# Kernel optimization log

Measured on AMD Instinct MI355X. Metric: run time of the kernel, lower is better.

The kernel has to match this reference:

```python
import jax, jax.numpy as jnp
import numpy as np

B, NBLK, D, DY, NDIM, NMC, DH = 4096, 12, 2, 2, 24, 256, 100
SQRT3 = 3.0 ** 0.5
G2 = np.array([[1.0, 0.0], [0.5, SQRT3 / 2.0]], dtype=np.float32)
G = jnp.asarray(np.kron(np.eye(NBLK, dtype=np.float32), G2))  # (24,24) block-diag hexagonal generator
LOG_VOL = (NDIM // 2) * float(np.log(SQRT3 / 2.0))  # log sqrt(det(G G^T))


def _lin(x, w, b=None):
    y = x @ w.T
    return y if b is None else y + b


def _hex_quantize(y):
    # Exact nearest-point quantizer for the product-of-A2 (hexagonal) lattice.
    p = y.reshape(y.shape[:-1] + (NDIM // 2, 2))
    off = jnp.array([0.5, SQRT3 / 2.0], dtype=y.dtype)
    def rnd(q):  # round to rectangular sublattice Z x sqrt(3)Z
        return jnp.stack([jnp.round(q[..., 0]), jnp.round(q[..., 1] / SQRT3) * SQRT3], axis=-1)
    c0 = rnd(p)
    c1 = rnd(p - off) + off
    d0 = jnp.sum((p - c0) ** 2, axis=-1)
    d1 = jnp.sum((p - c1) ** 2, axis=-1)
    return jnp.where((d0 <= d1)[..., None], c0, c1).reshape(y.shape)


def _logits_cumulative(v, Hs, bs, fs):
    # compressai-style per-channel monotone cumulative network. v: (..., C) -> (..., C)
    v = v[..., None]  # (..., C, 1)
    for k in range(len(Hs)):
        v = jnp.einsum('coi,...ci->...co', jax.nn.softplus(Hs[k]), v) + bs[k][:, :, 0]
        if k < len(fs):
            v = v + jnp.tanh(fs[k][:, :, 0]) * jnp.tanh(v)
    return v[..., 0]


def setup_inputs() -> dict:
    key = jax.random.key(0)
    ks = iter(jax.random.split(key, 64))
    def nrm(shape, s=1.0):
        return jax.random.normal(next(ks), shape, jnp.float32) * s
    inp = {}
    inp['x'] = nrm((B, NBLK, D))
    inp['y_mean'] = nrm((NBLK, DY))
    inp['u'] = jax.random.uniform(next(ks), (NMC, NDIM), jnp.float32)
    inp['ga_w0'] = nrm((DH, D), D ** -0.5); inp['ga_b0'] = jnp.zeros((DH,), jnp.float32)
    inp['ga_w1'] = nrm((DH, DH), DH ** -0.5); inp['ga_b1'] = jnp.zeros((DH,), jnp.float32)
    inp['ga_w2'] = nrm((DY, DH), DH ** -0.5); inp['ga_b2'] = jnp.zeros((DY,), jnp.float32)
    inp['gs_w0'] = nrm((DH, DY), DY ** -0.5); inp['gs_b0'] = jnp.zeros((DH,), jnp.float32)
    inp['gs_w1'] = nrm((DH, DH), DH ** -0.5); inp['gs_b1'] = jnp.zeros((DH,), jnp.float32)
    inp['gs_w2'] = nrm((D, DH), DH ** -0.5); inp['gs_b2'] = jnp.zeros((D,), jnp.float32)
    inp['gac_w0'] = nrm((DH, NDIM), NDIM ** -0.5)
    inp['gac_w1'] = nrm((DH, DH), DH ** -0.5)
    inp['gac_w2'] = nrm((NDIM, DH), DH ** -0.5)
    inp['gsc_w0'] = nrm((DH, NDIM), NDIM ** -0.5)
    inp['gsc_w1'] = nrm((DH, DH), DH ** -0.5)
    inp['gsc_w2'] = nrm((NDIM, DH), DH ** -0.5)
    # factorized-prior cumulative params, layer dims 1->3->3->3->3->1
    inp['eb_H0'] = nrm((NDIM, 3, 1), 0.5)
    inp['eb_H1'] = nrm((NDIM, 3, 3), 0.5)
    inp['eb_H2'] = nrm((NDIM, 3, 3), 0.5)
    inp['eb_H3'] = nrm((NDIM, 3, 3), 0.5)
    inp['eb_H4'] = nrm((NDIM, 1, 3), 0.5)
    inp['eb_b0'] = nrm((NDIM, 3, 1), 0.5)
    inp['eb_b1'] = nrm((NDIM, 3, 1), 0.5)
    inp['eb_b2'] = nrm((NDIM, 3, 1), 0.5)
    inp['eb_b3'] = nrm((NDIM, 3, 1), 0.5)
    inp['eb_b4'] = nrm((NDIM, 1, 1), 0.5)
    inp['eb_a0'] = nrm((NDIM, 3, 1), 0.5)
    inp['eb_a1'] = nrm((NDIM, 3, 1), 0.5)
    inp['eb_a2'] = nrm((NDIM, 3, 1), 0.5)
    inp['eb_a3'] = nrm((NDIM, 3, 1), 0.5)
    return inp


def reference(x, y_mean, u, ga_w0, ga_b0, ga_w1, ga_b1, ga_w2, ga_b2,
              gs_w0, gs_b0, gs_w1, gs_b1, gs_w2, gs_b2,
              gac_w0, gac_w1, gac_w2, gsc_w0, gsc_w1, gsc_w2,
              eb_H0, eb_H1, eb_H2, eb_H3, eb_H4,
              eb_b0, eb_b1, eb_b2, eb_b3, eb_b4,
              eb_a0, eb_a1, eb_a2, eb_a3):
    lrelu, sp = jax.nn.leaky_relu, jax.nn.softplus
    # analysis transform g_a: (B, 12, 2) -> (B, 12, dy)
    y1 = _lin(lrelu(_lin(lrelu(_lin(x, ga_w0, ga_b0)), ga_w1, ga_b1)), ga_w2, ga_b2)
    # EMA zero-mean update (buffer assignment => no gradient through the mean)
    ym = jax.lax.stop_gradient(0.05 * y_mean + 0.95 * jnp.mean(y1, axis=0))
    y1 = (y1 - ym).reshape(B, NDIM)
    # coupled analysis transform g_a_c (Softplus MLP, no bias)
    y1 = _lin(sp(_lin(sp(_lin(y1, gac_w0)), gac_w1)), gac_w2)
    # quasi-uniform samples from the Voronoi cell of the lattice origin
    u2 = u @ G
    u2 = u2 - _hex_quantize(u2)
    # lattice quantization with straight-through estimator
    y_q = _hex_quantize(y1)
    y_hat = y1 + jax.lax.stop_gradient(y_q - y1)
    # Monte-Carlo log-likelihood over the Voronoi cell with factorized prior density
    Hs = (eb_H0, eb_H1, eb_H2, eb_H3, eb_H4)
    bs = (eb_b0, eb_b1, eb_b2, eb_b3, eb_b4)
    fs = (eb_a0, eb_a1, eb_a2, eb_a3)
    pts = y_hat[:, None, :] + u2[None, :, :]  # (B, NMC, NDIM)
    def cdf(p):
        return jax.nn.sigmoid(_logits_cumulative(p, Hs, bs, fs))
    _, pdf = jax.jvp(cdf, (pts,), (jnp.ones_like(pts),))  # density = d/dx cdf(x)
    logp = jnp.sum(jnp.log(pdf + 1e-9), axis=-1)  # (B, NMC)
    lik = jax.scipy.special.logsumexp(logp, axis=1) - jnp.log(jnp.float32(NMC)) + LOG_VOL  # (B,)
    # synthesis transforms
    y_hat1 = _lin(sp(_lin(sp(_lin(y_hat, gsc_w0)), gsc_w1)), gsc_w2).reshape(B, NBLK, DY) + ym
    x_hat = _lin(lrelu(_lin(lrelu(_lin(y_hat1, gs_w0, gs_b0)), gs_w1, gs_b1)), gs_w2, gs_b2)
    return (x_hat, lik)
```

## Files before the change

### kernel.cpp

```cpp
#include <hip/hip_runtime.h>
#include <hip/hip_bf16.h>
#include <math.h>
#include <limits.h>

constexpr int NB    = 4096;
constexpr int ROWS2 = NB * 12;
constexpr int G2_BLOCKS = ROWS2 / 64;
constexpr int TBL_CAP = 64;
constexpr int KBASE   = -32;

constexpr size_t WS_Y1    = 0;
constexpr size_t WS_YHAT  = 98304;
constexpr size_t WS_YHAT1 = 196608;
constexpr size_t WS_YM    = 294912;
constexpr size_t WS_U2T   = 294936;
constexpr size_t WS_EB    = 301080;
constexpr size_t WS_PART  = 302472;
constexpr size_t WS_W1T   = 320904;
constexpr size_t WS_TBL   = 372104;
constexpr size_t WS_END   = WS_TBL + 24 * TBL_CAP * 256;

constexpr float STEP_ODD = 0.8660254037844386f;
constexpr float INV_ODD  = 1.1547005383792517f;

__device__ __forceinline__ float lrelu(float x) { return x >= 0.f ? x : 0.01f * x; }
__device__ __forceinline__ float rcp_fast(float x) { return __builtin_amdgcn_rcpf(x); }

__device__ __forceinline__ float tanh_fast(float x) {
    float xx = fminf(fmaxf(x, -15.f), 15.f);
    float e = __expf(xx + xx);
    return fmaf(-2.f, rcp_fast(e + 1.f), 1.f);
}
__device__ __forceinline__ float splus(float x) {
    return fmaxf(x, 0.f) + __logf(1.f + __expf(-fabsf(x)));
}
__device__ __forceinline__ float splus_precise(float x) {
    return fmaxf(x, 0.f) + log1pf(expf(-fabsf(x)));
}

__device__ __forceinline__ void fma4(float4& a, float h, const float4& w) {
    a.x = fmaf(h, w.x, a.x); a.y = fmaf(h, w.y, a.y);
    a.z = fmaf(h, w.z, a.z); a.w = fmaf(h, w.w, a.w);
}

__device__ __forceinline__ void hexq(float p0, float p1, float& q0, float& q1) {
    const float S3 = 1.7320508075688772f;
    const float H3 = 0.8660254037844386f;
    float c00 = rintf(p0);
    float c01 = rintf(p1 / S3) * S3;
    float c10 = rintf(p0 - 0.5f) + 0.5f;
    float c11 = rintf((p1 - H3) / S3) * S3 + H3;
    float d0 = (p0 - c00) * (p0 - c00) + (p1 - c01) * (p1 - c01);
    float d1 = (p0 - c10) * (p0 - c10) + (p1 - c11) * (p1 - c11);
    bool take0 = d0 <= d1;
    q0 = take0 ? c00 : c10;
    q1 = take0 ? c01 : c11;
}

__device__ __forceinline__ float logpdf_ch(const float* __restrict__ P, float p) {
    float w00 = P[0], w01 = P[1], w02 = P[2];
    float z0 = fmaf(w00, p, P[3]);
    float z1 = fmaf(w01, p, P[4]);
    float z2 = fmaf(w02, p, P[5]);
    float a0 = P[6], a1 = P[7], a2 = P[8];
    float e0 = tanh_fast(z0), e1 = tanh_fast(z1), e2 = tanh_fast(z2);
    float h0 = fmaf(a0, e0, z0), h1 = fmaf(a1, e1, z1), h2 = fmaf(a2, e2, z2);
    float t0 = w00 * fmaf(a0, fmaf(-e0, e0, 1.f), 1.f);
    float t1 = w01 * fmaf(a1, fmaf(-e1, e1, 1.f), 1.f);
    float t2 = w02 * fmaf(a2, fmaf(-e2, e2, 1.f), 1.f);

#define EB_LAYER(O)                                                            \
    {                                                                          \
        float z0n = fmaf(P[O+0], h0, fmaf(P[O+1], h1, fmaf(P[O+2], h2, P[O+9])));  \
        float z1n = fmaf(P[O+3], h0, fmaf(P[O+4], h1, fmaf(P[O+5], h2, P[O+10]))); \
        float z2n = fmaf(P[O+6], h0, fmaf(P[O+7], h1, fmaf(P[O+8], h2, P[O+11]))); \
        float s0 = fmaf(P[O+0], t0, fmaf(P[O+1], t1, P[O+2] * t2));            \
        float s1 = fmaf(P[O+3], t0, fmaf(P[O+4], t1, P[O+5] * t2));            \
        float s2 = fmaf(P[O+6], t0, fmaf(P[O+7], t1, P[O+8] * t2));            \
        float g0 = P[O+12], g1 = P[O+13], g2 = P[O+14];                        \
        float q0 = tanh_fast(z0n), q1 = tanh_fast(z1n), q2 = tanh_fast(z2n);   \
        h0 = fmaf(g0, q0, z0n); h1 = fmaf(g1, q1, z1n); h2 = fmaf(g2, q2, z2n); \
        t0 = s0 * fmaf(g0, fmaf(-q0, q0, 1.f), 1.f);                           \
        t1 = s1 * fmaf(g1, fmaf(-q1, q1, 1.f), 1.f);                           \
        t2 = s2 * fmaf(g2, fmaf(-q2, q2, 1.f), 1.f);                           \
    }
    EB_LAYER(9)
    EB_LAYER(24)
    EB_LAYER(39)
#undef EB_LAYER

    float L = fmaf(P[54], h0, fmaf(P[55], h1, fmaf(P[56], h2, P[57])));
    float T = fmaf(P[54], t0, fmaf(P[55], t1, P[56] * t2));
    float Lc = fminf(fmaxf(L, -30.f), 30.f);
    float sg = rcp_fast(1.f + __expf(-Lc));
    float pdf = sg * (1.f - sg) * T;
    return __logf(pdf + 1e-9f);
}

__global__ __launch_bounds__(256) void k_prep(
    const float* __restrict__ H0p, const float* __restrict__ H1p,
    const float* __restrict__ H2p, const float* __restrict__ H3p,
    const float* __restrict__ H4p,
    const float* __restrict__ b0p, const float* __restrict__ b1p,
    const float* __restrict__ b2p, const float* __restrict__ b3p,
    const float* __restrict__ b4p,
    const float* __restrict__ a0p, const float* __restrict__ a1p,
    const float* __restrict__ a2p, const float* __restrict__ a3p,
    const float* __restrict__ u,
    const float* __restrict__ w1ga, const float* __restrict__ w1gac,
    const float* __restrict__ w1gsc, const float* __restrict__ w1gs,
    float* __restrict__ eb, float* __restrict__ u2t,
    float* __restrict__ w1t)
{
    int tid = threadIdx.x;
    if (blockIdx.x > 0) {
        int t = blockIdx.x - 1;
        int m = t / 50;
        int o = (t % 50) * 256 + tid;
        int k = o >> 7, i = o & 127;
        const float* src = (m == 0) ? w1ga : (m == 1) ? w1gac
                         : (m == 2) ? w1gsc : w1gs;
        w1t[m * 12800 + o] = (i < 100) ? src[i * 100 + k] : 0.f;
        return;
    }
    if (tid < 24) {
        int c = tid;
        float* P = eb + c * 58;
        for (int j = 0; j < 3; ++j) P[j]      = splus_precise(H0p[c*3+j]);
        for (int j = 0; j < 3; ++j) P[3+j]    = b0p[c*3+j];
        for (int j = 0; j < 3; ++j) P[6+j]    = tanhf(a0p[c*3+j]);
        for (int j = 0; j < 9; ++j) P[9+j]    = splus_precise(H1p[c*9+j]);
        for (int j = 0; j < 3; ++j) P[18+j]   = b1p[c*3+j];
        for (int j = 0; j < 3; ++j) P[21+j]   = tanhf(a1p[c*3+j]);
        for (int j = 0; j < 9; ++j) P[24+j]   = splus_precise(H2p[c*9+j]);
        for (int j = 0; j < 3; ++j) P[33+j]   = b2p[c*3+j];
        for (int j = 0; j < 3; ++j) P[36+j]   = tanhf(a2p[c*3+j]);
        for (int j = 0; j < 9; ++j) P[39+j]   = splus_precise(H3p[c*9+j]);
        for (int j = 0; j < 3; ++j) P[48+j]   = b3p[c*3+j];
        for (int j = 0; j < 3; ++j) P[51+j]   = tanhf(a3p[c*3+j]);
        for (int j = 0; j < 3; ++j) P[54+j]   = splus_precise(H4p[c*3+j]);
        P[57] = b4p[c];
    }
    int m = tid;
    if (m < 256) {
        for (int j = 0; j < 12; ++j) {
            float a  = u[m*24 + 2*j];
            float bb = u[m*24 + 2*j + 1];
            float p0 = fmaf(0.5f, bb, a);
            float p1 = 0.8660254037844386f * bb;
            float q0, q1; hexq(p0, p1, q0, q1);
            u2t[(2*j)   * 256 + m] = p0 - q0;
            u2t[(2*j+1) * 256 + m] = p1 - q1;
        }
    }
}

template <int MEAN>
__device__ __forceinline__ void gemm2_body(
    int bid,
    const float* __restrict__ in,
    const float* __restrict__ w0, const float* __restrict__ b0,
    const float* __restrict__ w1t,
    const float* __restrict__ b1, const float* __restrict__ w2,
    const float* __restrict__ b2,
    float* __restrict__ out, float* __restrict__ partial)
{
    __shared__ alignas(16) float shT[100 * 64];
    __shared__ float S[64][2];

    int tid = threadIdx.x;
    int row0 = bid * 64;

    int lrow = tid & 63, jg = tid >> 6;
    float2 xv = ((const float2*)in)[row0 + lrow];
#pragma unroll
    for (int jj = 0; jj < 25; ++jj) {
        int j = jg * 25 + jj;
        shT[j * 64 + lrow] =
            lrelu(fmaf(w0[2*j], xv.x, fmaf(w0[2*j+1], xv.y, b0[j])));
    }

    int lane = tid & 63, wv = tid >> 6;
    int ct = lane & 31;
    int rt = wv * 2 + (lane >> 5);
    bool cvalid = (4 * ct < 100);
    float4 zero4 = make_float4(0.f, 0.f, 0.f, 0.f);
    float4 b14 = cvalid ? *(const float4*)(b1 + 4*ct) : zero4;
    float4 w20 = cvalid ? *(const float4*)(w2 + 4*ct) : zero4;
    float4 w21 = cvalid ? *(const float4*)(w2 + 100 + 4*ct) : zero4;
    __syncthreads();

    float4 acc[8];
#pragma unroll
    for (int r = 0; r < 8; ++r) acc[r] = zero4;
    const float4* wg  = (const float4*)w1t + ct;
    const float4* hT4 = (const float4*)shT;
#pragma unroll 4
    for (int k = 0; k < 100; ++k) {
        float4 w4 = wg[k * 32];
        float4 ha = hT4[k * 16 + rt * 2];
        float4 hb = hT4[k * 16 + rt * 2 + 1];
        fma4(acc[0], ha.x, w4); fma4(acc[1], ha.y, w4);
        fma4(acc[2], ha.z, w4); fma4(acc[3], ha.w, w4);
        fma4(acc[4], hb.x, w4); fma4(acc[5], hb.y, w4);
        fma4(acc[6], hb.z, w4); fma4(acc[7], hb.w, w4);
    }
    __syncthreads();

    float* red = shT;
#pragma unroll
    for (int r = 0; r < 8; ++r) {
        float a0 = lrelu(acc[r].x + b14.x);
        float a1 = lrelu(acc[r].y + b14.y);
        float a2 = lrelu(acc[r].z + b14.z);
        float a3 = lrelu(acc[r].w + b14.w);
        float y0 = fmaf(a0, w20.x, fmaf(a1, w20.y, fmaf(a2, w20.z, a3 * w20.w)));
        float y1 = fmaf(a0, w21.x, fmaf(a1, w21.y, fmaf(a2, w21.z, a3 * w21.w)));
        int row = rt * 8 + r;
        red[(row * 2) * 32 + ct]     = y0;
        red[(row * 2 + 1) * 32 + ct] = y1;
    }
    __syncthreads();
    if (tid < 128) {
        int row = tid >> 1, p = tid & 1;
        const float4* rp = (const float4*)&red[(row * 2 + p) * 32];
        float s = 0.f;
#pragma unroll
        for (int g = 0; g < 8; ++g) {
            float4 v = rp[g];
            s += (v.x + v.y) + (v.z + v.w);
        }
        float y = s + b2[p];
        out[(row0 + row) * 2 + p] = y;
        if (MEAN) S[row][p] = y;
    }
    if (MEAN) {
        __syncthreads();
        if (tid < 24) {
            int j = tid >> 1, par = tid & 1;
            int base = row0 % 12;
            int k0 = (j - base + 12) % 12;
            float s = 0.f;
            for (int k = k0; k < 64; k += 12) s += S[k][par];
            partial[bid * 24 + tid] = s;
        }
    }
}

__global__ __launch_bounds__(256, 4) void k_ga_table(
    const float* __restrict__ in,
    const float* __restrict__ w0, const float* __restrict__ b0,
    const float* __restrict__ w1t,
    const float* __restrict__ b1, const float* __restrict__ w2,
    const float* __restrict__ b2,
    float* __restrict__ out, float* __restrict__ partial,
    const float* __restrict__ eb, const float* __restrict__ u2t,
    float* __restrict__ tbl)
{
    if (blockIdx.x < (unsigned)G2_BLOCKS) {
        gemm2_body<1>(blockIdx.x, in, w0, b0, w1t, b1, w2, b2, out, partial);
    } else {
        int cv = blockIdx.x - G2_BLOCKS;
        int c = cv >> 6, v = cv & 63;
        int m = threadIdx.x;
        float step = (c & 1) ? STEP_ODD : 0.5f;
        float val = (float)(KBASE + v) * step;
        float p = val + u2t[c * 256 + m];
        tbl[cv * 256 + m] = logpdf_ch(eb + c * 58, p);
    }
}

__global__ __launch_bounds__(256) void k_mean_final(
    const float* __restrict__ partial, const float* __restrict__ y_mean,
    float* __restrict__ ym)
{
    int tid = threadIdx.x;
    int c = tid >> 3, s = tid & 7;
    float v = 0.f;
    if (c < 24)
        for (int g = s; g < G2_BLOCKS; g += 8) v += partial[g * 24 + c];
    v += __shfl_xor(v, 1); v += __shfl_xor(v, 2); v += __shfl_xor(v, 4);
    if (c < 24 && s == 0)
        ym[c] = fmaf(0.05f, y_mean[c], 0.95f * (v * (1.0f / NB)));
}

__global__ __launch_bounds__(256, 4) void k_fused24(
    const float* __restrict__ y1,
    const float* __restrict__ w0A, const float* __restrict__ w1tA,
    const float* __restrict__ w2A,
    const float* __restrict__ w0B, const float* __restrict__ w1tB,
    const float* __restrict__ w2B,
    const float* __restrict__ ymg,
    float* __restrict__ yhat, float* __restrict__ yhat1)
{
    __shared__ float sw0[2400];
    __shared__ float sw2[2400];
    __shared__ float sX[8 * 25];
    __shared__ float sO[8 * 25];
    __shared__ alignas(16) float h0[100 * 8];
    __shared__ float h1[100 * 8];
    __shared__ float symL[24];

    int tid = threadIdx.x;
    int row0 = blockIdx.x * 8;

    if (tid < 24) symL[tid] = ymg[tid];
    __syncthreads();
    for (int e = tid; e < 192; e += 256) {
        int r = e / 24, c = e - r * 24;
        sX[r * 25 + c] = y1[row0 * 24 + e] - symL[c];
    }

    int ii = tid & 127, rg = tid >> 7;

    for (int pass = 0; pass < 2; ++pass) {
        const float* w0  = pass ? w0B  : w0A;
        const float* w1t = pass ? w1tB : w1tA;
        const float* w2  = pass ? w2B  : w2A;
        for (int t = tid; t < 2400; t += 256) {
            sw0[t] = w0[t];
            sw2[t] = w2[t];
        }
        __syncthreads();

        for (int e = tid; e < 800; e += 256) {
            int j = e >> 3, r = e & 7;
            const float* wr = sw0 + j * 24;
            const float* xr = sX + r * 25;
            float a = 0.f, b = 0.f;
#pragma unroll
            for (int k = 0; k < 24; k += 2) {
                a = fmaf(wr[k],     xr[k],     a);
                b = fmaf(wr[k + 1], xr[k + 1], b);
            }
            h0[j * 8 + r] = splus(a + b);
        }
        __syncthreads();

        {
            float4 a = make_float4(0.f, 0.f, 0.f, 0.f);
            const float* wc = w1t + ii;
            const float4* h4 = (const float4*)h0 + rg;
#pragma unroll 4
            for (int j = 0; j < 100; ++j) {
                float w = wc[j * 128];
                float4 h = h4[j * 2];
                a.x = fmaf(w, h.x, a.x); a.y = fmaf(w, h.y, a.y);
                a.z = fmaf(w, h.z, a.z); a.w = fmaf(w, h.w, a.w);
            }
            if (ii < 100) {
                h1[ii * 8 + rg * 4]     = splus(a.x);
                h1[ii * 8 + rg * 4 + 1] = splus(a.y);
                h1[ii * 8 + rg * 4 + 2] = splus(a.z);
                h1[ii * 8 + rg * 4 + 3] = splus(a.w);
            }
        }
        __syncthreads();

        if (tid < 192) {
            int c = tid >> 3, r = tid & 7;
            const float* w2r = sw2 + c * 100;
            float s = 0.f, s2 = 0.f;
#pragma unroll 4
            for (int i = 0; i < 100; i += 2) {
                s  = fmaf(w2r[i],     h1[i * 8 + r],       s);
                s2 = fmaf(w2r[i + 1], h1[(i + 1) * 8 + r], s2);
            }
            float v = s + s2;
            if (pass == 0) sO[r * 25 + c] = v;
            else yhat1[(row0 + r) * 24 + c] = v + symL[c];
        }

        if (pass == 0) {
            __syncthreads();
            if (tid < 96) {
                int pr = tid >> 3, r = tid & 7;
                float v0 = sO[r * 25 + 2*pr], v1 = sO[r * 25 + 2*pr + 1];
                float q0, q1; hexq(v0, v1, q0, q1);
                yhat[(row0 + r) * 24 + 2*pr]     = q0;
                yhat[(row0 + r) * 24 + 2*pr + 1] = q1;
                sX[r * 25 + 2*pr]     = q0;
                sX[r * 25 + 2*pr + 1] = q1;
            }
        }
    }
}

__global__ __launch_bounds__(256, 4) void k_gs(
    const float* __restrict__ yhat1,
    const float* __restrict__ w0, const float* __restrict__ b0,
    const float* __restrict__ w1t,
    const float* __restrict__ b1, const float* __restrict__ w2,
    const float* __restrict__ b2, float* __restrict__ xhat)
{
    gemm2_body<0>(blockIdx.x, yhat1, w0, b0, w1t, b1, w2, b2, xhat, nullptr);
}

__global__ __launch_bounds__(256) void k_mc_tbl(
    const float* __restrict__ yhat, const float* __restrict__ u2t,
    const float* __restrict__ eb,
    const float* __restrict__ tbl, float* __restrict__ lik)
{
    __shared__ float redm[4], reds[4];
    int tid = threadIdx.x;
    int wv = tid >> 6;
    int b = blockIdx.x;

    float y[24];
    const float4* yr = (const float4*)(yhat + b * 24);
#pragma unroll
    for (int k4 = 0; k4 < 6; ++k4) {
        float4 t = yr[k4];
        y[4*k4] = t.x; y[4*k4+1] = t.y; y[4*k4+2] = t.z; y[4*k4+3] = t.w;
    }

    float lp = 0.f;
    unsigned miss = 0;
#pragma unroll
    for (int c = 0; c < 24; ++c) {
        float inv = (c & 1) ? INV_ODD : 2.0f;
        int k = (int)rintf(y[c] * inv);
        int idx = k - KBASE;
        if (idx >= 0 && idx < TBL_CAP)
            lp += tbl[(c * TBL_CAP + idx) * 256 + tid];
        else
            miss |= (1u << c);
    }
    while (miss) {
        int c = __ffs(miss) - 1;
        miss &= miss - 1;
        lp += logpdf_ch(eb + c * 58, y[c] + u2t[c * 256 + tid]);
    }

    float m = lp;
#pragma unroll
    for (int off = 1; off < 64; off <<= 1) m = fmaxf(m, __shfl_xor(m, off));
    if ((tid & 63) == 0) redm[wv] = m;
    __syncthreads();
    float mx = fmaxf(fmaxf(redm[0], redm[1]), fmaxf(redm[2], redm[3]));
    float e = __expf(lp - mx);
#pragma unroll
    for (int off = 1; off < 64; off <<= 1) e += __shfl_xor(e, off);
    if ((tid & 63) == 0) reds[wv] = e;
    __syncthreads();
    if (tid == 0)
        lik[b] = mx + __logf(reds[0] + reds[1] + reds[2] + reds[3])
               - 7.271269879190247f;
}

__global__ __launch_bounds__(256) void k_mc_direct(
    const float* __restrict__ yhat, const float* __restrict__ u2t,
    const float* __restrict__ eb, float* __restrict__ lik)
{
    __shared__ alignas(16) float sU[24 * 256];
    __shared__ float redm[4], reds[4];
    int tid = threadIdx.x;
    int wv = tid >> 6;
    int b = blockIdx.x;
    for (int i = tid; i < 1536; i += 256)
        ((float4*)sU)[i] = ((const float4*)u2t)[i];
    __syncthreads();

    float lp = 0.f;
    for (int c = 0; c < 24; ++c)
        lp += logpdf_ch(eb + c * 58, yhat[b * 24 + c] + sU[c * 256 + tid]);

    float m = lp;
#pragma unroll
    for (int off = 1; off < 64; off <<= 1) m = fmaxf(m, __shfl_xor(m, off));
    if ((tid & 63) == 0) redm[wv] = m;
    __syncthreads();
    float mx = fmaxf(fmaxf(redm[0], redm[1]), fmaxf(redm[2], redm[3]));
    float e = __expf(lp - mx);
#pragma unroll
    for (int off = 1; off < 64; off <<= 1) e += __shfl_xor(e, off);
    if ((tid & 63) == 0) reds[wv] = e;
    __syncthreads();
    if (tid == 0)
        lik[b] = mx + __logf(reds[0] + reds[1] + reds[2] + reds[3])
               - 7.271269879190247f;
}

extern "C" void kernel_launch(void* const* d_in, const int* in_sizes, int n_in,
                              void* d_out, int out_size, void* d_ws, size_t ws_size,
                              hipStream_t stream)
{
    (void)in_sizes; (void)n_in; (void)out_size;
    const float* x      = (const float*)d_in[0];
    const float* y_mean = (const float*)d_in[1];
    const float* u      = (const float*)d_in[2];
    const float* ga_w0  = (const float*)d_in[3];
    const float* ga_b0  = (const float*)d_in[4];
    const float* ga_w1  = (const float*)d_in[5];
    const float* ga_b1  = (const float*)d_in[6];
    const float* ga_w2  = (const float*)d_in[7];
    const float* ga_b2  = (const float*)d_in[8];
    const float* gs_w0  = (const float*)d_in[9];
    const float* gs_b0  = (const float*)d_in[10];
    const float* gs_w1  = (const float*)d_in[11];
    const float* gs_b1  = (const float*)d_in[12];
    const float* gs_w2  = (const float*)d_in[13];
    const float* gs_b2  = (const float*)d_in[14];
    const float* gac_w0 = (const float*)d_in[15];
    const float* gac_w1 = (const float*)d_in[16];
    const float* gac_w2 = (const float*)d_in[17];
    const float* gsc_w0 = (const float*)d_in[18];
    const float* gsc_w1 = (const float*)d_in[19];
    const float* gsc_w2 = (const float*)d_in[20];
    const float* eb_H0  = (const float*)d_in[21];
    const float* eb_H1  = (const float*)d_in[22];
    const float* eb_H2  = (const float*)d_in[23];
    const float* eb_H3  = (const float*)d_in[24];
    const float* eb_H4  = (const float*)d_in[25];
    const float* eb_b0  = (const float*)d_in[26];
    const float* eb_b1  = (const float*)d_in[27];
    const float* eb_b2  = (const float*)d_in[28];
    const float* eb_b3  = (const float*)d_in[29];
    const float* eb_b4  = (const float*)d_in[30];
    const float* eb_a0  = (const float*)d_in[31];
    const float* eb_a1  = (const float*)d_in[32];
    const float* eb_a2  = (const float*)d_in[33];
    const float* eb_a3  = (const float*)d_in[34];

    float* ws    = (float*)d_ws;
    float* y1    = ws + WS_Y1;
    float* yhat  = ws + WS_YHAT;
    float* yhat1 = ws + WS_YHAT1;
    float* ym    = ws + WS_YM;
    float* u2t   = ws + WS_U2T;
    float* eb    = ws + WS_EB;
    float* part  = ws + WS_PART;
    float* w1t   = ws + WS_W1T;
    float* tbl   = ws + WS_TBL;
    float* xhat  = (float*)d_out;
    float* lik   = (float*)d_out + 98304;

    float* w1tGA  = w1t;
    float* w1tGAC = w1t + 12800;
    float* w1tGSC = w1t + 25600;
    float* w1tGS  = w1t + 38400;

    bool use_tbl = ws_size >= WS_END * sizeof(float);

    k_prep<<<201, 256, 0, stream>>>(eb_H0, eb_H1, eb_H2, eb_H3, eb_H4,
                                    eb_b0, eb_b1, eb_b2, eb_b3, eb_b4,
                                    eb_a0, eb_a1, eb_a2, eb_a3, u,
                                    ga_w1, gac_w1, gsc_w1, gs_w1,
                                    eb, u2t, w1t);
    if (use_tbl)
        k_ga_table<<<G2_BLOCKS + 24 * TBL_CAP, 256, 0, stream>>>(
            x, ga_w0, ga_b0, w1tGA, ga_b1, ga_w2, ga_b2, y1, part,
            eb, u2t, tbl);
    else
        k_ga_table<<<G2_BLOCKS, 256, 0, stream>>>(
            x, ga_w0, ga_b0, w1tGA, ga_b1, ga_w2, ga_b2, y1, part,
            eb, u2t, tbl);
    k_mean_final<<<1, 256, 0, stream>>>(part, y_mean, ym);
    k_fused24<<<NB / 8, 256, 0, stream>>>(y1, gac_w0, w1tGAC, gac_w2,
                                          gsc_w0, w1tGSC, gsc_w2,
                                          ym, yhat, yhat1);
    k_gs<<<G2_BLOCKS, 256, 0, stream>>>(yhat1, gs_w0, gs_b0, w1tGS,
                                        gs_b1, gs_w2, gs_b2, xhat);
    if (use_tbl)
        k_mc_tbl<<<NB, 256, 0, stream>>>(yhat, u2t, eb, tbl, lik);
    else
        k_mc_direct<<<NB, 256, 0, stream>>>(yhat, u2t, eb, lik);
}
```

Baseline: 131.9 us.

## Merge gs and MC kernels, read fused24 weights untransposed, prefetch w1 in gemm

The synthesis gemm kernel and the table-based Monte-Carlo likelihood kernel are merged into one launch, with blocks split by block index, so the two independent stages share the grid and one launch is saved. k_fused24 now reads the gac/gsc hidden weights row-major as float4 directly instead of using prep-transposed copies, which halves the transpose work in k_prep. The shared gemm loop prefetches weights two iterations ahead. Risks: the merged kernel's launch bounds (256,4) now also apply to the MC path, and the fused24 layer-1 loop leaves threads with ii>=100 idle.

```diff
diff --git a/kernel.cpp b/kernel.cpp
--- a/kernel.cpp
+++ b/kernel.cpp
@@ -107,8 +107,7 @@
     const float* __restrict__ a0p, const float* __restrict__ a1p,
     const float* __restrict__ a2p, const float* __restrict__ a3p,
     const float* __restrict__ u,
-    const float* __restrict__ w1ga, const float* __restrict__ w1gac,
-    const float* __restrict__ w1gsc, const float* __restrict__ w1gs,
+    const float* __restrict__ w1ga, const float* __restrict__ w1gs,
     float* __restrict__ eb, float* __restrict__ u2t,
     float* __restrict__ w1t)
 {
@@ -118,8 +117,7 @@
         int m = t / 50;
         int o = (t % 50) * 256 + tid;
         int k = o >> 7, i = o & 127;
-        const float* src = (m == 0) ? w1ga : (m == 1) ? w1gac
-                         : (m == 2) ? w1gsc : w1gs;
+        const float* src = (m == 0) ? w1ga : w1gs;
         w1t[m * 12800 + o] = (i < 100) ? src[i * 100 + k] : 0.f;
         return;
     }
@@ -195,15 +193,18 @@
     for (int r = 0; r < 8; ++r) acc[r] = zero4;
     const float4* wg  = (const float4*)w1t + ct;
     const float4* hT4 = (const float4*)shT;
+    float4 wa = wg[0];
+    float4 wb = wg[32];
 #pragma unroll 4
     for (int k = 0; k < 100; ++k) {
-        float4 w4 = wg[k * 32];
+        float4 wn = wg[(k + 2) * 32];
         float4 ha = hT4[k * 16 + rt * 2];
         float4 hb = hT4[k * 16 + rt * 2 + 1];
-        fma4(acc[0], ha.x, w4); fma4(acc[1], ha.y, w4);
-        fma4(acc[2], ha.z, w4); fma4(acc[3], ha.w, w4);
-        fma4(acc[4], hb.x, w4); fma4(acc[5], hb.y, w4);
-        fma4(acc[6], hb.z, w4); fma4(acc[7], hb.w, w4);
+        fma4(acc[0], ha.x, wa); fma4(acc[1], ha.y, wa);
+        fma4(acc[2], ha.z, wa); fma4(acc[3], ha.w, wa);
+        fma4(acc[4], hb.x, wa); fma4(acc[5], hb.y, wa);
+        fma4(acc[6], hb.z, wa); fma4(acc[7], hb.w, wa);
+        wa = wb; wb = wn;
     }
     __syncthreads();
 
@@ -286,9 +287,9 @@
 
 __global__ __launch_bounds__(256, 4) void k_fused24(
     const float* __restrict__ y1,
-    const float* __restrict__ w0A, const float* __restrict__ w1tA,
+    const float* __restrict__ w0A, const float* __restrict__ w1A,
     const float* __restrict__ w2A,
-    const float* __restrict__ w0B, const float* __restrict__ w1tB,
+    const float* __restrict__ w0B, const float* __restrict__ w1B,
     const float* __restrict__ w2B,
     const float* __restrict__ ymg,
     float* __restrict__ yhat, float* __restrict__ yhat1)
@@ -315,7 +316,7 @@
 
     for (int pass = 0; pass < 2; ++pass) {
         const float* w0  = pass ? w0B  : w0A;
-        const float* w1t = pass ? w1tB : w1tA;
+        const float* w1  = pass ? w1B  : w1A;
         const float* w2  = pass ? w2B  : w2A;
         for (int t = tid; t < 2400; t += 256) {
             sw0[t] = w0[t];
@@ -337,23 +338,26 @@
         }
         __syncthreads();
 
-        {
+        if (ii < 100) {
             float4 a = make_float4(0.f, 0.f, 0.f, 0.f);
-            const float* wc = w1t + ii;
+            const float4* wr = (const float4*)(w1 + ii * 100);
             const float4* h4 = (const float4*)h0 + rg;
-#pragma unroll 4
-            for (int j = 0; j < 100; ++j) {
-                float w = wc[j * 128];
-                float4 h = h4[j * 2];
-                a.x = fmaf(w, h.x, a.x); a.y = fmaf(w, h.y, a.y);
-                a.z = fmaf(w, h.z, a.z); a.w = fmaf(w, h.w, a.w);
+#pragma unroll 5
+            for (int j4 = 0; j4 < 25; ++j4) {
+                float4 wv = wr[j4];
+                float4 ha = h4[(4*j4)     * 2];
+                float4 hb = h4[(4*j4 + 1) * 2];
+                float4 hc = h4[(4*j4 + 2) * 2];
+                float4 hd = h4[(4*j4 + 3) * 2];
+                fma4(a, wv.x, ha);
+                fma4(a, wv.y, hb);
+                fma4(a, wv.z, hc);
+                fma4(a, wv.w, hd);
             }
-            if (ii < 100) {
-                h1[ii * 8 + rg * 4]     = splus(a.x);
-                h1[ii * 8 + rg * 4 + 1] = splus(a.y);
-                h1[ii * 8 + rg * 4 + 2] = splus(a.z);
-                h1[ii * 8 + rg * 4 + 3] = splus(a.w);
-            }
+            h1[ii * 8 + rg * 4]     = splus(a.x);
+            h1[ii * 8 + rg * 4 + 1] = splus(a.y);
+            h1[ii * 8 + rg * 4 + 2] = splus(a.z);
+            h1[ii * 8 + rg * 4 + 3] = splus(a.w);
         }
         __syncthreads();
 
@@ -386,25 +390,24 @@
     }
 }
 
-__global__ __launch_bounds__(256, 4) void k_gs(
+__global__ __launch_bounds__(256, 4) void k_gs_mc(
     const float* __restrict__ yhat1,
     const float* __restrict__ w0, const float* __restrict__ b0,
     const float* __restrict__ w1t,
     const float* __restrict__ b1, const float* __restrict__ w2,
-    const float* __restrict__ b2, float* __restrict__ xhat)
-{
-    gemm2_body<0>(blockIdx.x, yhat1, w0, b0, w1t, b1, w2, b2, xhat, nullptr);
-}
-
-__global__ __launch_bounds__(256) void k_mc_tbl(
+    const float* __restrict__ b2, float* __restrict__ xhat,
     const float* __restrict__ yhat, const float* __restrict__ u2t,
     const float* __restrict__ eb,
     const float* __restrict__ tbl, float* __restrict__ lik)
 {
+    if (blockIdx.x < (unsigned)G2_BLOCKS) {
+        gemm2_body<0>(blockIdx.x, yhat1, w0, b0, w1t, b1, w2, b2, xhat, nullptr);
+        return;
+    }
     __shared__ float redm[4], reds[4];
     int tid = threadIdx.x;
     int wv = tid >> 6;
-    int b = blockIdx.x;
+    int b = blockIdx.x - G2_BLOCKS;
 
     float y[24];
     const float4* yr = (const float4*)(yhat + b * 24);
@@ -446,6 +449,16 @@
     if (tid == 0)
         lik[b] = mx + __logf(reds[0] + reds[1] + reds[2] + reds[3])
                - 7.271269879190247f;
+}
+
+__global__ __launch_bounds__(256, 4) void k_gs(
+    const float* __restrict__ yhat1,
+    const float* __restrict__ w0, const float* __restrict__ b0,
+    const float* __restrict__ w1t,
+    const float* __restrict__ b1, const float* __restrict__ w2,
+    const float* __restrict__ b2, float* __restrict__ xhat)
+{
+    gemm2_body<0>(blockIdx.x, yhat1, w0, b0, w1t, b1, w2, b2, xhat, nullptr);
 }
 
 __global__ __launch_bounds__(256) void k_mc_direct(
@@ -535,18 +548,15 @@
     float* xhat  = (float*)d_out;
     float* lik   = (float*)d_out + 98304;
 
-    float* w1tGA  = w1t;
-    float* w1tGAC = w1t + 12800;
-    float* w1tGSC = w1t + 25600;
-    float* w1tGS  = w1t + 38400;
+    float* w1tGA = w1t;
+    float* w1tGS = w1t + 12800;
 
     bool use_tbl = ws_size >= WS_END * sizeof(float);
 
-    k_prep<<<201, 256, 0, stream>>>(eb_H0, eb_H1, eb_H2, eb_H3, eb_H4,
+    k_prep<<<101, 256, 0, stream>>>(eb_H0, eb_H1, eb_H2, eb_H3, eb_H4,
                                     eb_b0, eb_b1, eb_b2, eb_b3, eb_b4,
                                     eb_a0, eb_a1, eb_a2, eb_a3, u,
-                                    ga_w1, gac_w1, gsc_w1, gs_w1,
-                                    eb, u2t, w1t);
+                                    ga_w1, gs_w1, eb, u2t, w1t);
     if (use_tbl)
         k_ga_table<<<G2_BLOCKS + 24 * TBL_CAP, 256, 0, stream>>>(
             x, ga_w0, ga_b0, w1tGA, ga_b1, ga_w2, ga_b2, y1, part,
@@ -556,13 +566,16 @@
             x, ga_w0, ga_b0, w1tGA, ga_b1, ga_w2, ga_b2, y1, part,
             eb, u2t, tbl);
     k_mean_final<<<1, 256, 0, stream>>>(part, y_mean, ym);
-    k_fused24<<<NB / 8, 256, 0, stream>>>(y1, gac_w0, w1tGAC, gac_w2,
-                                          gsc_w0, w1tGSC, gsc_w2,
+    k_fused24<<<NB / 8, 256, 0, stream>>>(y1, gac_w0, gac_w1, gac_w2,
+                                          gsc_w0, gsc_w1, gsc_w2,
                                           ym, yhat, yhat1);
-    k_gs<<<G2_BLOCKS, 256, 0, stream>>>(yhat1, gs_w0, gs_b0, w1tGS,
-                                        gs_b1, gs_w2, gs_b2, xhat);
-    if (use_tbl)
-        k_mc_tbl<<<NB, 256, 0, stream>>>(yhat, u2t, eb, tbl, lik);
-    else
+    if (use_tbl) {
+        k_gs_mc<<<G2_BLOCKS + NB, 256, 0, stream>>>(
+            yhat1, gs_w0, gs_b0, w1tGS, gs_b1, gs_w2, gs_b2, xhat,
+            yhat, u2t, eb, tbl, lik);
+    } else {
+        k_gs<<<G2_BLOCKS, 256, 0, stream>>>(
+            yhat1, gs_w0, gs_b0, w1tGS, gs_b1, gs_w2, gs_b2, xhat);
         k_mc_direct<<<NB, 256, 0, stream>>>(yhat, u2t, eb, lik);
-}
+    }
+}
```

Result: faster. 121.3 us (-8.0%).

## Fuse synthesis GEMM with table-based MC likelihood and batch table builds

Applied to the files above, without the earlier changes.

Merges the k_gs synthesis MLP and the table-lookup Monte-Carlo likelihood kernel into one launch. Each MC block now handles four batch rows and does branchless clamped table loads. The table-build blocks now compute four table entries each, so there are a quarter as many blocks. The gemm inner loop adds a four-deep register prefetch of weight rows to hide global load latency. Trade-offs: an extra kernel-launch boundary is removed and more work is shared per block, but MC blocks now serialise four rows with extra barriers, and the prefetch reads past row 99 of the transposed weights.

```diff
diff --git a/kernel.cpp b/kernel.cpp
--- a/kernel.cpp
+++ b/kernel.cpp
@@ -195,15 +195,20 @@
     for (int r = 0; r < 8; ++r) acc[r] = zero4;
     const float4* wg  = (const float4*)w1t + ct;
     const float4* hT4 = (const float4*)shT;
+    float4 wq0 = wg[0], wq1 = wg[32], wq2 = wg[64], wq3 = wg[96];
 #pragma unroll 4
     for (int k = 0; k < 100; ++k) {
-        float4 w4 = wg[k * 32];
+        float4 wcur;
+        if ((k & 3) == 0)      { wcur = wq0; wq0 = wg[(k + 4) * 32]; }
+        else if ((k & 3) == 1) { wcur = wq1; wq1 = wg[(k + 4) * 32]; }
+        else if ((k & 3) == 2) { wcur = wq2; wq2 = wg[(k + 4) * 32]; }
+        else                   { wcur = wq3; wq3 = wg[(k + 4) * 32]; }
         float4 ha = hT4[k * 16 + rt * 2];
         float4 hb = hT4[k * 16 + rt * 2 + 1];
-        fma4(acc[0], ha.x, w4); fma4(acc[1], ha.y, w4);
-        fma4(acc[2], ha.z, w4); fma4(acc[3], ha.w, w4);
-        fma4(acc[4], hb.x, w4); fma4(acc[5], hb.y, w4);
-        fma4(acc[6], hb.z, w4); fma4(acc[7], hb.w, w4);
+        fma4(acc[0], ha.x, wcur); fma4(acc[1], ha.y, wcur);
+        fma4(acc[2], ha.z, wcur); fma4(acc[3], ha.w, wcur);
+        fma4(acc[4], hb.x, wcur); fma4(acc[5], hb.y, wcur);
+        fma4(acc[6], hb.z, wcur); fma4(acc[7], hb.w, wcur);
     }
     __syncthreads();
 
@@ -260,13 +265,18 @@
     if (blockIdx.x < (unsigned)G2_BLOCKS) {
         gemm2_body<1>(blockIdx.x, in, w0, b0, w1t, b1, w2, b2, out, partial);
     } else {
-        int cv = blockIdx.x - G2_BLOCKS;
-        int c = cv >> 6, v = cv & 63;
+        int cv4 = blockIdx.x - G2_BLOCKS;
+        int c = cv4 >> 4, vg = (cv4 & 15) * 4;
         int m = threadIdx.x;
         float step = (c & 1) ? STEP_ODD : 0.5f;
-        float val = (float)(KBASE + v) * step;
-        float p = val + u2t[c * 256 + m];
-        tbl[cv * 256 + m] = logpdf_ch(eb + c * 58, p);
+        float uv = u2t[c * 256 + m];
+        const float* P = eb + c * 58;
+#pragma unroll
+        for (int dv = 0; dv < 4; ++dv) {
+            int v = vg + dv;
+            float val = (float)(KBASE + v) * step;
+            tbl[(c * TBL_CAP + v) * 256 + m] = logpdf_ch(P, val + uv);
+        }
     }
 }
 
@@ -386,6 +396,68 @@
     }
 }
 
+__global__ __launch_bounds__(256, 4) void k_gs_mc(
+    const float* __restrict__ yhat1,
+    const float* __restrict__ w0, const float* __restrict__ b0,
+    const float* __restrict__ w1t,
+    const float* __restrict__ b1, const float* __restrict__ w2,
+    const float* __restrict__ b2, float* __restrict__ xhat,
+    const float* __restrict__ yhat, const float* __restrict__ u2t,
+    const float* __restrict__ eb,
+    const float* __restrict__ tbl, float* __restrict__ lik)
+{
+    if (blockIdx.x < (unsigned)G2_BLOCKS) {
+        gemm2_body<0>(blockIdx.x, yhat1, w0, b0, w1t, b1, w2, b2, xhat, nullptr);
+        return;
+    }
+    __shared__ float sy[4 * 24];
+    __shared__ float redm[4], reds[4];
+    int tid = threadIdx.x;
+    int wv = tid >> 6;
+    int bg = (blockIdx.x - G2_BLOCKS) * 4;
+
+    if (tid < 96) sy[tid] = yhat[bg * 24 + tid];
+    __syncthreads();
+
+    for (int q = 0; q < 4; ++q) {
+        float lp = 0.f;
+        unsigned miss = 0;
+#pragma unroll
+        for (int c = 0; c < 24; ++c) {
+            float yv = sy[q * 24 + c];
+            float inv = (c & 1) ? INV_ODD : 2.0f;
+            int k = (int)rintf(yv * inv);
+            int idx = k - KBASE;
+            bool ok = (idx >= 0 && idx < TBL_CAP);
+            int idq = min(max(idx, 0), TBL_CAP - 1);
+            float tv = tbl[(c * TBL_CAP + idq) * 256 + tid];
+            lp += ok ? tv : 0.f;
+            if (!ok) miss |= (1u << c);
+        }
+        while (miss) {
+            int c = __ffs(miss) - 1;
+            miss &= miss - 1;
+            lp += logpdf_ch(eb + c * 58, sy[q * 24 + c] + u2t[c * 256 + tid]);
+        }
+
+        float m = lp;
+#pragma unroll
+        for (int off = 1; off < 64; off <<= 1) m = fmaxf(m, __shfl_xor(m, off));
+        if ((tid & 63) == 0) redm[wv] = m;
+        __syncthreads();
+        float mx = fmaxf(fmaxf(redm[0], redm[1]), fmaxf(redm[2], redm[3]));
+        float e = __expf(lp - mx);
+#pragma unroll
+        for (int off = 1; off < 64; off <<= 1) e += __shfl_xor(e, off);
+        if ((tid & 63) == 0) reds[wv] = e;
+        __syncthreads();
+        if (tid == 0)
+            lik[bg + q] = mx + __logf(reds[0] + reds[1] + reds[2] + reds[3])
+                        - 7.271269879190247f;
+        __syncthreads();
+    }
+}
+
 __global__ __launch_bounds__(256, 4) void k_gs(
     const float* __restrict__ yhat1,
     const float* __restrict__ w0, const float* __restrict__ b0,
@@ -394,58 +466,6 @@
     const float* __restrict__ b2, float* __restrict__ xhat)
 {
     gemm2_body<0>(blockIdx.x, yhat1, w0, b0, w1t, b1, w2, b2, xhat, nullptr);
-}
-
-__global__ __launch_bounds__(256) void k_mc_tbl(
-    const float* __restrict__ yhat, const float* __restrict__ u2t,
-    const float* __restrict__ eb,
-    const float* __restrict__ tbl, float* __restrict__ lik)
-{
-    __shared__ float redm[4], reds[4];
-    int tid = threadIdx.x;
-    int wv = tid >> 6;
-    int b = blockIdx.x;
-
-    float y[24];
-    const float4* yr = (const float4*)(yhat + b * 24);
-#pragma unroll
-    for (int k4 = 0; k4 < 6; ++k4) {
-        float4 t = yr[k4];
-        y[4*k4] = t.x; y[4*k4+1] = t.y; y[4*k4+2] = t.z; y[4*k4+3] = t.w;
-    }
-
-    float lp = 0.f;
-    unsigned miss = 0;
-#pragma unroll
-    for (int c = 0; c < 24; ++c) {
-        float inv = (c & 1) ? INV_ODD : 2.0f;
-        int k = (int)rintf(y[c] * inv);
-        int idx = k - KBASE;
-        if (idx >= 0 && idx < TBL_CAP)
-            lp += tbl[(c * TBL_CAP + idx) * 256 + tid];
-        else
-            miss |= (1u << c);
-    }
-    while (miss) {
-        int c = __ffs(miss) - 1;
-        miss &= miss - 1;
-        lp += logpdf_ch(eb + c * 58, y[c] + u2t[c * 256 + tid]);
-    }
-
-    float m = lp;
-#pragma unroll
-    for (int off = 1; off < 64; off <<= 1) m = fmaxf(m, __shfl_xor(m, off));
-    if ((tid & 63) == 0) redm[wv] = m;
-    __syncthreads();
-    float mx = fmaxf(fmaxf(redm[0], redm[1]), fmaxf(redm[2], redm[3]));
-    float e = __expf(lp - mx);
-#pragma unroll
-    for (int off = 1; off < 64; off <<= 1) e += __shfl_xor(e, off);
-    if ((tid & 63) == 0) reds[wv] = e;
-    __syncthreads();
-    if (tid == 0)
-        lik[b] = mx + __logf(reds[0] + reds[1] + reds[2] + reds[3])
-               - 7.271269879190247f;
 }
 
 __global__ __launch_bounds__(256) void k_mc_direct(
@@ -548,7 +568,7 @@
                                     ga_w1, gac_w1, gsc_w1, gs_w1,
                                     eb, u2t, w1t);
     if (use_tbl)
-        k_ga_table<<<G2_BLOCKS + 24 * TBL_CAP, 256, 0, stream>>>(
+        k_ga_table<<<G2_BLOCKS + 24 * TBL_CAP / 4, 256, 0, stream>>>(
             x, ga_w0, ga_b0, w1tGA, ga_b1, ga_w2, ga_b2, y1, part,
             eb, u2t, tbl);
     else
@@ -559,10 +579,13 @@
     k_fused24<<<NB / 8, 256, 0, stream>>>(y1, gac_w0, w1tGAC, gac_w2,
                                           gsc_w0, w1tGSC, gsc_w2,
                                           ym, yhat, yhat1);
-    k_gs<<<G2_BLOCKS, 256, 0, stream>>>(yhat1, gs_w0, gs_b0, w1tGS,
-                                        gs_b1, gs_w2, gs_b2, xhat);
-    if (use_tbl)
-        k_mc_tbl<<<NB, 256, 0, stream>>>(yhat, u2t, eb, tbl, lik);
-    else
+    if (use_tbl) {
+        k_gs_mc<<<G2_BLOCKS + NB / 4, 256, 0, stream>>>(
+            yhat1, gs_w0, gs_b0, w1tGS, gs_b1, gs_w2, gs_b2, xhat,
+            yhat, u2t, eb, tbl, lik);
+    } else {
+        k_gs<<<G2_BLOCKS, 256, 0, stream>>>(
+            yhat1, gs_w0, gs_b0, w1tGS, gs_b1, gs_w2, gs_b2, xhat);
         k_mc_direct<<<NB, 256, 0, stream>>>(yhat, u2t, eb, lik);
-}
+    }
+}
```

Result: faster. 123.8 us (-6.1%).
